# Kernel optimization log

Measured on AMD Instinct MI355X. Metric: run time of the kernel, lower is better.

Reference implementation:

```python
import jax, jax.numpy as jnp
import numpy as np

B, NPG, IN_DIM, H, E = 128, 500, 3, 128, 512000
N = B * NPG
NEG = -1e9  # stands in for -inf masked fill; exp underflows to exactly 0 in fp32
BN_EPS = 1e-5


def setup_inputs() -> dict:
    key = jax.random.key(0)
    ks = jax.random.split(key, 40)
    rn = lambda k, shape: (jax.random.normal(k, shape, jnp.float32) * 0.05)
    x = jax.random.normal(ks[0], (N, IN_DIM), jnp.float32)
    g = jax.random.randint(ks[1], (E,), 0, B)
    src = jax.random.randint(ks[2], (E,), 0, NPG) + g * NPG
    dst = jax.random.randint(ks[3], (E,), 0, NPG) + g * NPG
    edge_index = jnp.stack([src, dst]).astype(jnp.int32)
    batch = (jnp.arange(N) // NPG).astype(jnp.int32)
    feasible_mask = jax.random.uniform(ks[4], (B, NPG, NPG)) < 0.1
    feasible_mask = feasible_mask.at[:, 0, 0].set(True)  # >=1 feasible action/graph
    return dict(
        x=x, edge_index=edge_index, batch=batch, feasible_mask=feasible_mask,
        gin_W1_0=rn(ks[5], (IN_DIM, H)), gin_b1_0=jnp.zeros((H,), jnp.float32),
        gin_g_0=jnp.ones((H,), jnp.float32), gin_be_0=jnp.zeros((H,), jnp.float32),
        gin_W2_0=rn(ks[6], (H, H)), gin_b2_0=jnp.zeros((H,), jnp.float32),
        gin_W1=rn(ks[7], (3, H, H)), gin_b1=jnp.zeros((3, H), jnp.float32),
        gin_g=jnp.ones((3, H), jnp.float32), gin_be=jnp.zeros((3, H), jnp.float32),
        gin_W2=rn(ks[8], (3, H, H)), gin_b2=jnp.zeros((3, H), jnp.float32),
        pol_W1_0=rn(ks[9], (2 * H, H)), pol_b1_0=jnp.zeros((H,), jnp.float32),
        pol_W2_0=rn(ks[10], (H, H)), pol_b2_0=jnp.zeros((H,), jnp.float32),
        pol_W1=rn(ks[11], (2, H, H)), pol_b1=jnp.zeros((2, H), jnp.float32),
        pol_W2=rn(ks[12], (2, H, H)), pol_b2=jnp.zeros((2, H), jnp.float32),
    )


def _gin_conv(h, src, dst, deg, W1, b1, g, be, W2, b2):
    # mean-aggregate neighbors (self loops already in edge list), eps=0
    agg = jax.ops.segment_sum(h[src], dst, num_segments=N) / deg[:, None]
    z = (h + agg) @ W1 + b1
    mu = jnp.mean(z, axis=0)
    var = jnp.var(z, axis=0)  # biased var, as torch BN training mode
    z = (z - mu) * jax.lax.rsqrt(var + BN_EPS) * g + be
    return jax.nn.relu(z) @ W2 + b2


def reference(x, edge_index, batch, feasible_mask,
              gin_W1_0, gin_b1_0, gin_g_0, gin_be_0, gin_W2_0, gin_b2_0,
              gin_W1, gin_b1, gin_g, gin_be, gin_W2, gin_b2,
              pol_W1_0, pol_b1_0, pol_W2_0, pol_b2_0,
              pol_W1, pol_b1, pol_W2, pol_b2):
    # add self loops
    loop = jnp.arange(N, dtype=edge_index.dtype)
    src = jnp.concatenate([edge_index[0], loop])
    dst = jnp.concatenate([edge_index[1], loop])
    deg = jnp.maximum(jax.ops.segment_sum(jnp.ones_like(src, jnp.float32), dst, num_segments=N), 1.0)

    h = _gin_conv(x, src, dst, deg, gin_W1_0, gin_b1_0, gin_g_0, gin_be_0, gin_W2_0, gin_b2_0)
    node_pool = h
    graph_pool = jax.ops.segment_sum(h, batch, num_segments=B) / NPG
    for l in range(3):
        h = _gin_conv(h, src, dst, deg, gin_W1[l], gin_b1[l], gin_g[l], gin_be[l], gin_W2[l], gin_b2[l])
        node_pool = node_pool + h
        graph_pool = graph_pool + jax.ops.segment_sum(h, batch, num_segments=B) / NPG

    # augment node embeds with their graph embed (graphs contiguous, equal size)
    a = jnp.concatenate([node_pool, graph_pool[batch]], axis=-1).reshape(B, NPG, 2 * H)
    a = jnp.tanh(a @ pol_W1_0 + pol_b1_0) @ pol_W2_0 + pol_b2_0
    for l in range(2):
        a = jnp.tanh(a @ pol_W1[l] + pol_b1[l]) @ pol_W2[l] + pol_b2[l]

    scores = jnp.einsum('bnd,bmd->bnm', a, a)                 # [B, n, n]
    scores = jnp.where(feasible_mask, scores, NEG)
    flat = scores.reshape(B, NPG * NPG)
    logp_all = jax.nn.log_softmax(flat, axis=-1)
    actions_id = jax.random.categorical(jax.random.key(42), flat, axis=-1)  # [B]
    log_prob = jnp.take_along_axis(logp_all, actions_id[:, None], axis=1)[:, 0]
    return actions_id, log_prob
```

## Files before the change

### kernel.cpp

```cpp
#include <hip/hip_runtime.h>
#include <float.h>

#define NN 64000
#define BB 128
#define NPGc 500
#define EE 512000

#define SKW(c) ((c) + (((c)>>3)<<2))
#define LW 188

__device__ __forceinline__ unsigned rotl32(unsigned x, unsigned r){ return (x<<r)|(x>>(32u-r)); }

__device__ __forceinline__ unsigned threefry_bits(unsigned idx){
  unsigned x0 = 0u, x1 = idx;
  const unsigned ks0 = 0u, ks1 = 42u, ks2 = 0u ^ 42u ^ 0x1BD11BDAu;
  x0 += ks0; x1 += ks1;
#define RND(r) { x0 += x1; x1 = rotl32(x1, r); x1 ^= x0; }
  RND(13u) RND(15u) RND(26u) RND(6u)   x0 += ks1; x1 += ks2 + 1u;
  RND(17u) RND(29u) RND(16u) RND(24u)  x0 += ks2; x1 += ks0 + 2u;
  RND(13u) RND(15u) RND(26u) RND(6u)   x0 += ks0; x1 += ks1 + 3u;
  RND(17u) RND(29u) RND(16u) RND(24u)  x0 += ks1; x1 += ks2 + 4u;
  RND(13u) RND(15u) RND(26u) RND(6u)   x0 += ks2; x1 += ks0 + 5u;
#undef RND
  return x0 ^ x1;
}

__device__ __forceinline__ float gumbel_of(unsigned idx){
  unsigned bits = threefry_bits(idx);
  float f = __uint_as_float((bits >> 9) | 0x3f800000u) - 1.0f;
  const float TINY = 1.17549435e-38f;
  float u = fmaxf(TINY, f + TINY);
  return -logf(-logf(u));
}

__device__ __forceinline__ float fast_tanh(float x){
  return 1.0f - 2.0f/(__expf(2.0f*x) + 1.0f);
}

__global__ void maskdet_kernel(const unsigned* __restrict__ m, int* __restrict__ flag){
  if (threadIdx.x == 0){
    int isbool = 0;
    for (int i=0;i<256;i++){ if (m[i] > 1u){ isbool = 1; break; } }
    *flag = isbool;
  }
}

__global__ __launch_bounds__(256)
void maskprep_kernel(const unsigned char* __restrict__ mu8src, const int* __restrict__ mi32src,
                     const int* __restrict__ mflag, unsigned char* __restrict__ mn8,
                     unsigned char* __restrict__ mt8){
  __shared__ unsigned char tile[64][65];
  const int b = blockIdx.y;
  const int rt = blockIdx.x >> 3, ct = blockIdx.x & 7;
  const int t = threadIdx.x;
  const int lane = t & 63, rr = t >> 6;
  const int isbool = *mflag;
#pragma unroll
  for (int p=0;p<16;p++){
    int row = rt*64 + p*4 + rr;
    int col = ct*64 + lane;
    unsigned char v = 0;
    if (row < NPGc && col < NPGc){
      size_t off = (size_t)b*250000 + (size_t)row*500 + col;
      v = isbool ? mu8src[off] : (unsigned char)(mi32src[off] != 0);
      mn8[off] = v;
    }
    tile[p*4+rr][lane] = v;
  }
  __syncthreads();
#pragma unroll
  for (int p=0;p<16;p++){
    int orow = ct*64 + p*4 + rr;
    int ocol = rt*64 + lane;
    if (orow < NPGc && ocol < NPGc){
      size_t off = (size_t)b*250000 + (size_t)orow*500 + ocol;
      mt8[off] = tile[lane][p*4+rr];
    }
  }
}

__global__ void count_kernel(const int* __restrict__ dst, int* __restrict__ cnt){
  int e = blockIdx.x*256 + threadIdx.x;
  if (e < EE) atomicAdd(&cnt[dst[e]], 1);
}

__global__ void scanA_kernel(const int* __restrict__ cnt, int* __restrict__ bsum){
  __shared__ int red[256];
  int t = threadIdx.x;
  red[t] = cnt[blockIdx.x*256 + t];
  __syncthreads();
  for (int s=128;s>0;s>>=1){
    if (t < s) red[t] += red[t+s];
    __syncthreads();
  }
  if (t == 0) bsum[blockIdx.x] = red[0];
}

__global__ void scanB_kernel(const int* __restrict__ bsum, int* __restrict__ boff){
  if (threadIdx.x == 0){
    int run = 0;
    for (int i=0;i<250;i++){ boff[i] = run; run += bsum[i]; }
    boff[250] = run;
  }
}

__global__ void scanC_kernel(const int* __restrict__ cnt, const int* __restrict__ boff,
                             int* __restrict__ off, int* __restrict__ cur){
  __shared__ int red[256];
  int t = threadIdx.x;
  int n = blockIdx.x*256 + t;
  int v = cnt[n];
  red[t] = v;
  __syncthreads();
  for (int d=1; d<256; d<<=1){
    int x = (t >= d) ? red[t-d] : 0;
    __syncthreads();
    red[t] += x;
    __syncthreads();
  }
  int excl = red[t] - v + boff[blockIdx.x];
  off[n] = excl; cur[n] = excl;
  if (n == NN-1) off[NN] = excl + v;
}

__global__ void fill_kernel(const int* __restrict__ src, const int* __restrict__ dst,
                            int* __restrict__ cur, int* __restrict__ csr){
  int e = blockIdx.x*256 + threadIdx.x;
  if (e < EE){
    int d = dst[e];
    int p = atomicAdd(&cur[d], 1);
    csr[p] = src[e];
  }
}

__global__ __launch_bounds__(256)
void agg128_kernel(const float* __restrict__ h, const int* __restrict__ off,
                   const int* __restrict__ csr, const int* __restrict__ cnt,
                   float* __restrict__ xin){
  const int nb = gridDim.x;
  const int per = nb >> 3;
  int bid = (blockIdx.x % 8)*per + (blockIdx.x >> 3);
  int w = (bid*256 + (int)threadIdx.x) >> 6;
  int lane = threadIdx.x & 63;
  if (w >= NN) return;
  const float* hn = h + (size_t)w*128;
  float a0 = hn[lane], a1 = hn[lane+64];
  float s0 = a0, s1 = a1;
  int e0 = off[w], e1 = off[w+1];
  for (int e = e0; e < e1; ++e){
    int s = csr[e];
    const float* hs = h + (size_t)s*128;
    s0 += hs[lane]; s1 += hs[lane+64];
  }
  float di = 1.0f/(float)(cnt[w]+1);
  xin[(size_t)w*128 + lane]      = a0 + s0*di;
  xin[(size_t)w*128 + lane + 64] = a1 + s1*di;
}

__global__ __launch_bounds__(256)
void z0_kernel(const float* __restrict__ x, const int* __restrict__ off,
               const int* __restrict__ csr, const int* __restrict__ cnt,
               const float* __restrict__ W, const float* __restrict__ bias,
               float* __restrict__ z, float* __restrict__ stats){
  __shared__ float xr[192];
  __shared__ float ssum[128], ssq[128];
  int t = threadIdx.x;
  int row0 = blockIdx.x*64;
  if (t < 192){
    int nl = t/3, f = t - nl*3;
    int n = row0 + nl;
    float a = x[n*3+f];
    float s = a;
    int e1 = off[n+1];
    for (int e = off[n]; e < e1; ++e) s += x[csr[e]*3 + f];
    float di = 1.0f/(float)(cnt[n]+1);
    xr[t] = a + s*di;
  }
  if (t < 128){ ssum[t]=0.f; ssq[t]=0.f; }
  int f = t & 127, rg = t >> 7;
  float w0 = W[f], w1 = W[128+f], w2 = W[256+f], bb = bias[f];
  __syncthreads();
  float s = 0.f, q = 0.f;
  for (int i=0;i<32;i++){
    int r = rg*32 + i;
    float y = bb + xr[r*3]*w0 + xr[r*3+1]*w1 + xr[r*3+2]*w2;
    z[(size_t)(row0+r)*128 + f] = y;
    s += y; q += y*y;
  }
  atomicAdd(&ssum[f], s); atomicAdd(&ssq[f], q);
  __syncthreads();
  if (t < 128){ atomicAdd(&stats[t], ssum[t]); atomicAdd(&stats[128+t], ssq[t]); }
}

__global__ void bnfin_kernel(float* __restrict__ stats, const float* __restrict__ g,
                             const float* __restrict__ be, float* __restrict__ bnbuf){
  int f = threadIdx.x;
  float mu  = stats[f]     * (1.0f/NN);
  float var = stats[128+f] * (1.0f/NN) - mu*mu;
  float rsv = rsqrtf(var + 1e-5f);
  float sc  = g[f]*rsv;
  bnbuf[f]      = sc;
  bnbuf[128+f]  = be[f] - mu*sc;
  stats[f] = 0.f; stats[128+f] = 0.f;
}

template<int K, bool CATF, bool BNF, bool TANHF, bool STATSF, int POOLM>
__global__ __launch_bounds__(256, 2)
void linear_kernel(const float* X, const float* __restrict__ X2,
                   const float* __restrict__ W, const float* __restrict__ bias,
                   float* Y,
                   const float* __restrict__ bnsc, const float* __restrict__ bnsh,
                   float* __restrict__ stats, float* __restrict__ pool){
  __shared__ __align__(16) float xs[32][LW];
  __shared__ __align__(16) float ws[32][LW];
  __shared__ float ssum[128], ssq[128];
  const int t = threadIdx.x;
  const int row0 = blockIdx.x*128;
  const int cg = t & 15, rg = t >> 4;
  const int c0 = cg*8, r0 = rg*8;
  const int skr0 = SKW(r0), skc0 = SKW(c0);
  float acc[8][8];
#pragma unroll
  for (int r=0;r<8;r++)
#pragma unroll
    for (int c=0;c<8;c++) acc[r][c]=0.f;
  if (STATSF && t < 128){ ssum[t]=0.f; ssq[t]=0.f; }

  for (int kc=0; kc<K; kc+=32){
    __syncthreads();
#pragma unroll
    for (int i=0;i<4;i++){
      int task = t + 256*i;
      int n = task >> 3, k4 = task & 7;
      int gk = kc + k4*4;
      int row = row0 + n;
      float4 v;
      if (CATF){
        if (gk < 128) v = *(const float4*)(X  + (size_t)row*128 + gk);
        else          v = *(const float4*)(X2 + (size_t)(row/NPGc)*128 + (gk-128));
      } else {
        v = *(const float4*)(X + (size_t)row*K + gk);
      }
      if (BNF){
        float4 sc4 = *(const float4*)(bnsc + gk);
        float4 sh4 = *(const float4*)(bnsh + gk);
        v.x = fmaxf(0.f, v.x*sc4.x + sh4.x);
        v.y = fmaxf(0.f, v.y*sc4.y + sh4.y);
        v.z = fmaxf(0.f, v.z*sc4.z + sh4.z);
        v.w = fmaxf(0.f, v.w*sc4.w + sh4.w);
      }
      int ns = SKW(n);
      xs[k4*4+0][ns] = v.x; xs[k4*4+1][ns] = v.y;
      xs[k4*4+2][ns] = v.z; xs[k4*4+3][ns] = v.w;
    }
#pragma unroll
    for (int i=0;i<4;i++){
      int task = t + 256*i;
      int k = task >> 5, c4 = task & 31;
      float4 v = *(const float4*)(W + (size_t)(kc+k)*128 + c4*4);
      *(float4*)&ws[k][c4*4 + ((c4>>1)<<2)] = v;
    }
    __syncthreads();
#pragma unroll
    for (int k=0;k<32;k++){
      float4 xa = *(const float4*)&xs[k][skr0];
      float4 xb = *(const float4*)&xs[k][skr0+4];
      float4 wa = *(const float4*)&ws[k][skc0];
      float4 wb = *(const float4*)&ws[k][skc0+4];
      float xv[8] = {xa.x,xa.y,xa.z,xa.w,xb.x,xb.y,xb.z,xb.w};
      float wv[8] = {wa.x,wa.y,wa.z,wa.w,wb.x,wb.y,wb.z,wb.w};
#pragma unroll
      for (int r=0;r<8;r++)
#pragma unroll
        for (int c=0;c<8;c++)
          acc[r][c] += xv[r]*wv[c];
    }
  }
  float4 ba = *(const float4*)(bias + c0);
  float4 bb2 = *(const float4*)(bias + c0 + 4);
  float bv[8] = {ba.x,ba.y,ba.z,ba.w,bb2.x,bb2.y,bb2.z,bb2.w};
  float sc8[8], sq8[8];
#pragma unroll
  for (int c=0;c<8;c++){ sc8[c]=0.f; sq8[c]=0.f; }
#pragma unroll
  for (int r=0;r<8;r++){
    int n = row0 + r0 + r;
    float y[8];
#pragma unroll
    for (int c=0;c<8;c++){
      float v = acc[r][c] + bv[c];
      if (TANHF) v = fast_tanh(v);
      y[c] = v;
    }
    float4 y0; y0.x=y[0]; y0.y=y[1]; y0.z=y[2]; y0.w=y[3];
    float4 y1; y1.x=y[4]; y1.y=y[5]; y1.z=y[6]; y1.w=y[7];
    *(float4*)(Y + (size_t)n*128 + c0)     = y0;
    *(float4*)(Y + (size_t)n*128 + c0 + 4) = y1;
    if (POOLM == 1){
      *(float4*)(pool + (size_t)n*128 + c0)     = y0;
      *(float4*)(pool + (size_t)n*128 + c0 + 4) = y1;
    } else if (POOLM == 2){
      float4 p0 = *(const float4*)(pool + (size_t)n*128 + c0);
      float4 p1 = *(const float4*)(pool + (size_t)n*128 + c0 + 4);
      p0.x+=y[0]; p0.y+=y[1]; p0.z+=y[2]; p0.w+=y[3];
      p1.x+=y[4]; p1.y+=y[5]; p1.z+=y[6]; p1.w+=y[7];
      *(float4*)(pool + (size_t)n*128 + c0)     = p0;
      *(float4*)(pool + (size_t)n*128 + c0 + 4) = p1;
    }
    if (STATSF){
#pragma unroll
      for (int c=0;c<8;c++){ sc8[c]+=y[c]; sq8[c]+=y[c]*y[c]; }
    }
  }
  if (STATSF){
#pragma unroll
    for (int c=0;c<8;c++){
      atomicAdd(&ssum[c0+c], sc8[c]);
      atomicAdd(&ssq[c0+c],  sq8[c]);
    }
    __syncthreads();
    if (t < 128){
      atomicAdd(&stats[t],     ssum[t]);
      atomicAdd(&stats[128+t], ssq[t]);
    }
  }
}

__global__ __launch_bounds__(512)
void gpool_kernel(const float* __restrict__ pool, float* __restrict__ gpool){
  __shared__ float red[4][128];
  int b = blockIdx.x;
  int f = threadIdx.x & 127, part = threadIdx.x >> 7;
  const float* p = pool + (size_t)b*NPGc*128 + f;
  int rbeg = part*125, rend = rbeg + 125;
  float s = 0.f;
  for (int i=rbeg;i<rend;i++) s += p[(size_t)i*128];
  red[part][f] = s;
  __syncthreads();
  if (part == 0){
    float tot = ((red[0][f] + red[1][f]) + red[2][f]) + red[3][f];
    gpool[(size_t)b*128 + f] = tot * (1.0f/NPGc);
  }
}

#define QCAP 1024
#define NPAIR 36

__global__ __launch_bounds__(256)
void scores_tri_kernel(const float* __restrict__ A, const unsigned char* __restrict__ mn8,
                       const unsigned char* __restrict__ mt8, float* __restrict__ partials){
  __shared__ __align__(16) float as[128][68];
  __shared__ __align__(16) float bs[32][68];
  __shared__ float qs[QCAP];
  __shared__ int   qi[QCAP];
  __shared__ int   qcnt;
  float* rm  = qs;
  float* rs_ = qs + 256;
  float* rv  = qs + 512;
  float* rsc = qs + 768;
  int*   ri  = qi;
  const int t = threadIdx.x;
  const int lane = t & 63;
  const int xcd = blockIdx.x & 7;
  const int within = blockIdx.x >> 3;
  const int b = xcd*16 + within/NPAIR;
  int pidx = within % NPAIR, tn = 0;
  while (pidx >= 8 - tn){ pidx -= 8 - tn; tn++; }
  const int tm = tn + pidx;
  const int pair = within % NPAIR;
  const bool diag = (tn == tm);
  const int n0 = tn*64, m0 = tm*64;
  const int cgc = t & 15, rgc = t >> 4;
  const int r0_ = rgc*4, c0 = cgc*4;
  const float* Ab = A + (size_t)b*NPGc*128;
  const unsigned gbase = (unsigned)b*250000u;
  if (t == 0) qcnt = 0;

#pragma unroll
  for (int i=0;i<32;i++){
    int idx = t + 256*i;
    int k = idx & 127, r = idx >> 7;
    int n = n0 + r;
    as[k][r] = (n < NPGc) ? Ab[(size_t)n*128 + k] : 0.f;
  }

  float acc[4][4];
#pragma unroll
  for (int i2=0;i2<4;i2++)
#pragma unroll
    for (int j=0;j<4;j++) acc[i2][j]=0.f;

  for (int kc=0;kc<4;kc++){
    __syncthreads();
#pragma unroll
    for (int i=0;i<8;i++){
      int idx = t + 256*i;
      int kk = idx & 31, c = idx >> 5;
      int m = m0 + c;
      bs[kk][c] = (m < NPGc) ? Ab[(size_t)m*128 + kc*32 + kk] : 0.f;
    }
    __syncthreads();
#pragma unroll
    for (int kk=0;kk<32;kk++){
      float4 av = *(const float4*)&as[kc*32+kk][r0_];
      float4 bv4 = *(const float4*)&bs[kk][c0];
      float a_[4] = {av.x,av.y,av.z,av.w};
      float b_[4] = {bv4.x,bv4.y,bv4.z,bv4.w};
#pragma unroll
      for (int i2=0;i2<4;i2++)
#pragma unroll
        for (int j=0;j<4;j++)
          acc[i2][j] += a_[i2]*b_[j];
    }
  }

  float mrun = -1e30f, srun = 0.f, bval = -FLT_MAX, bsc = 0.f;
  int bidx = 0x7FFFFFFF;
  const int mbase = m0 + c0;
  const bool colok = (mbase < NPGc);
#pragma unroll
  for (int i2=0;i2<4;i2++){
    int n = n0 + r0_ + i2;
    bool rowok = colok && (n < NPGc);
    bool fn[4] = {false,false,false,false};
    bool fm[4] = {false,false,false,false};
    if (rowok){
      size_t moff = (size_t)b*250000 + (size_t)n*500 + (size_t)mbase;
      uchar4 mk = *(const uchar4*)(mn8 + moff);
      fn[0]=mk.x!=0; fn[1]=mk.y!=0; fn[2]=mk.z!=0; fn[3]=mk.w!=0;
      uchar4 tk = *(const uchar4*)(mt8 + moff);
      fm[0]=tk.x!=0; fm[1]=tk.y!=0; fm[2]=tk.z!=0; fm[3]=tk.w!=0;
    }
    float cntj[4], sj[4];
    bool pn[4], pm[4];
#pragma unroll
    for (int j=0;j<4;j++){
      int m = mbase + j;
      bool mok = rowok && (m < NPGc);
      bool keep = mok && (!diag || m >= n);
      bool isde = (n == m);
      float cnt = 0.f; bool a1=false, a2=false;
      if (keep){
        if (isde){ cnt = fn[j] ? 1.f : 0.f; a1 = fn[j]; }
        else { cnt = (fn[j]?1.f:0.f) + (fm[j]?1.f:0.f); a1 = fn[j]; a2 = fm[j]; }
      }
      cntj[j]=cnt; pn[j]=a1; pm[j]=a2;
      sj[j] = (cnt > 0.f) ? acc[i2][j] : -1e30f;
    }
    float tmx = fmaxf(fmaxf(sj[0],sj[1]), fmaxf(sj[2],sj[3]));
    float nm = fmaxf(mrun, tmx);
    float add = 0.f;
#pragma unroll
    for (int j=0;j<4;j++) add += cntj[j]*__expf(sj[j] - nm);
    srun = srun*__expf(mrun - nm) + add;
    mrun = nm;
#pragma unroll
    for (int j=0;j<4;j++){
      int m = mbase + j;
      float s = acc[i2][j];
#pragma unroll
      for (int d=0;d<2;d++){
        bool want = d ? pm[j] : pn[j];
        unsigned long long mb = __ballot(want);
        if (mb){
          int cntw = __popcll(mb);
          int pos  = __popcll(mb & ((1ull<<lane)-1ull));
          int basew = 0;
          if (lane == 0) basew = atomicAdd(&qcnt, cntw);
          basew = __shfl(basew, 0);
          if (want){
            int lidx = d ? (m*500 + n) : (n*500 + m);
            int slot = basew + pos;
            if (slot < QCAP){ qs[slot] = s; qi[slot] = lidx; }
            else {
              float g = gumbel_of(gbase + (unsigned)lidx);
              float val = s + g;
              if (val > bval || (val == bval && lidx < bidx)){ bval = val; bidx = lidx; bsc = s; }
            }
          }
        }
      }
    }
  }
  __syncthreads();
  int qn = qcnt; if (qn > QCAP) qn = QCAP;
  for (int i = t; i < qn; i += 256){
    float s = qs[i]; int idx = qi[i];
    float g = gumbel_of(gbase + (unsigned)idx);
    float val = s + g;
    if (val > bval || (val == bval && idx < bidx)){ bval = val; bidx = idx; bsc = s; }
  }
  __syncthreads();
  rm[t]=mrun; rs_[t]=srun; rv[t]=bval; ri[t]=bidx; rsc[t]=bsc;
  __syncthreads();
  for (int offr=128; offr>0; offr>>=1){
    if (t < offr){
      float m1 = rm[t], s1 = rs_[t];
      float m2 = rm[t+offr], s2 = rs_[t+offr];
      float M = fmaxf(m1, m2);
      float S = s1*expf(m1-M) + s2*expf(m2-M);
      rm[t] = M; rs_[t] = S;
      float v2 = rv[t+offr]; int i2_ = ri[t+offr];
      if (v2 > rv[t] || (v2 == rv[t] && i2_ < ri[t])){ rv[t]=v2; ri[t]=i2_; rsc[t]=rsc[t+offr]; }
    }
    __syncthreads();
  }
  if (t == 0){
    float* p = partials + ((size_t)b*NPAIR + pair)*8;
    p[0]=rm[0]; p[1]=rs_[0]; p[2]=rv[0]; p[3]=(float)ri[0]; p[4]=rsc[0];
  }
}

__global__ void finalize_kernel(const float* __restrict__ partials, float* __restrict__ out){
  int b = threadIdx.x;
  float M = -1e30f, S = 0.f, BV = -FLT_MAX, BS = 0.f;
  int BI = 0x7FFFFFFF;
  for (int tp=0; tp<NPAIR; tp++){
    const float* p = partials + ((size_t)b*NPAIR + tp)*8;
    float m = p[0], s = p[1], v = p[2]; int i = (int)p[3]; float sc2 = p[4];
    float nM = fmaxf(M, m);
    S = S*expf(M-nM) + s*expf(m-nM);
    M = nM;
    if (v > BV || (v == BV && i < BI)){ BV = v; BI = i; BS = sc2; }
  }
  out[b]      = (float)BI;
  out[BB + b] = BS - (M + logf(S));
}

extern "C" void kernel_launch(void* const* d_in, const int* in_sizes, int n_in,
                              void* d_out, int out_size, void* d_ws, size_t ws_size,
                              hipStream_t stream){
  const float* x        = (const float*)d_in[0];
  const int*   eidx     = (const int*)d_in[1];
  const void*  maskp    = d_in[3];
  const float* gin_W1_0 = (const float*)d_in[4];
  const float* gin_b1_0 = (const float*)d_in[5];
  const float* gin_g_0  = (const float*)d_in[6];
  const float* gin_be_0 = (const float*)d_in[7];
  const float* gin_W2_0 = (const float*)d_in[8];
  const float* gin_b2_0 = (const float*)d_in[9];
  const float* gin_W1   = (const float*)d_in[10];
  const float* gin_b1   = (const float*)d_in[11];
  const float* gin_g    = (const float*)d_in[12];
  const float* gin_be   = (const float*)d_in[13];
  const float* gin_W2   = (const float*)d_in[14];
  const float* gin_b2   = (const float*)d_in[15];
  const float* pol_W1_0 = (const float*)d_in[16];
  const float* pol_b1_0 = (const float*)d_in[17];
  const float* pol_W2_0 = (const float*)d_in[18];
  const float* pol_b2_0 = (const float*)d_in[19];
  const float* pol_W1   = (const float*)d_in[20];
  const float* pol_b1   = (const float*)d_in[21];
  const float* pol_W2   = (const float*)d_in[22];
  const float* pol_b2   = (const float*)d_in[23];
  float* out = (float*)d_out;

  char* p = (char*)d_ws;
  auto carve = [&](size_t bytes) -> void* {
    void* r = (void*)p; p += (bytes + 255) & ~(size_t)255; return r;
  };
  float* hbuf  = (float*)carve((size_t)NN*128*4);
  float* xin   = (float*)carve((size_t)NN*128*4);
  float* pool  = (float*)carve((size_t)NN*128*4);
  float* gpool = (float*)carve((size_t)BB*128*4);
  float* stats = (float*)carve(256*4);
  float* bnbuf = (float*)carve(256*4);
  float* partials = (float*)carve((size_t)BB*NPAIR*8*4);
  int* cnt  = (int*)carve((size_t)NN*4);
  int* off  = (int*)carve((size_t)(NN+1)*4);
  int* cur  = (int*)carve((size_t)NN*4);
  int* csr  = (int*)carve((size_t)EE*4);
  int* bsum = (int*)carve(256*4);
  int* boff = (int*)carve(256*4);
  int* mflag = (int*)carve(256);
  unsigned char* mn8 = (unsigned char*)carve((size_t)BB*250000);
  unsigned char* mt8 = (unsigned char*)carve((size_t)BB*250000);

  const int* srcp = eidx;
  const int* dstp = eidx + EE;

  maskdet_kernel<<<1, 64, 0, stream>>>((const unsigned*)maskp, mflag);
  {
    dim3 mg(64, BB);
    maskprep_kernel<<<mg, 256, 0, stream>>>((const unsigned char*)maskp, (const int*)maskp,
                                            mflag, mn8, mt8);
  }

  hipMemsetAsync(cnt, 0, (size_t)NN*4, stream);
  count_kernel<<<(EE+255)/256, 256, 0, stream>>>(dstp, cnt);
  scanA_kernel<<<NN/256, 256, 0, stream>>>(cnt, bsum);
  scanB_kernel<<<1, 64, 0, stream>>>(bsum, boff);
  scanC_kernel<<<NN/256, 256, 0, stream>>>(cnt, boff, off, cur);
  fill_kernel<<<(EE+255)/256, 256, 0, stream>>>(srcp, dstp, cur, csr);

  hipMemsetAsync(stats, 0, 256*4, stream);
  z0_kernel<<<NN/64, 256, 0, stream>>>(x, off, csr, cnt, gin_W1_0, gin_b1_0, xin, stats);
  bnfin_kernel<<<1, 128, 0, stream>>>(stats, gin_g_0, gin_be_0, bnbuf);
  linear_kernel<128,false,true,false,false,1><<<NN/128, 256, 0, stream>>>(
      xin, nullptr, gin_W2_0, gin_b2_0, hbuf, bnbuf, bnbuf+128, nullptr, pool);

  for (int l=0; l<3; l++){
    agg128_kernel<<<NN/4, 256, 0, stream>>>(hbuf, off, csr, cnt, xin);
    linear_kernel<128,false,false,false,true,0><<<NN/128, 256, 0, stream>>>(
        xin, nullptr, gin_W1 + (size_t)l*16384, gin_b1 + l*128, xin,
        nullptr, nullptr, stats, nullptr);
    bnfin_kernel<<<1, 128, 0, stream>>>(stats, gin_g + l*128, gin_be + l*128, bnbuf);
    linear_kernel<128,false,true,false,false,2><<<NN/128, 256, 0, stream>>>(
        xin, nullptr, gin_W2 + (size_t)l*16384, gin_b2 + l*128, hbuf,
        bnbuf, bnbuf+128, nullptr, pool);
  }

  gpool_kernel<<<BB, 512, 0, stream>>>(pool, gpool);
  linear_kernel<256,true,false,true,false,0><<<NN/128, 256, 0, stream>>>(
      pool, gpool, pol_W1_0, pol_b1_0, hbuf, nullptr, nullptr, nullptr, nullptr);
  linear_kernel<128,false,false,false,false,0><<<NN/128, 256, 0, stream>>>(
      hbuf, nullptr, pol_W2_0, pol_b2_0, xin, nullptr, nullptr, nullptr, nullptr);
  linear_kernel<128,false,false,true,false,0><<<NN/128, 256, 0, stream>>>(
      xin, nullptr, pol_W1, pol_b1, hbuf, nullptr, nullptr, nullptr, nullptr);
  linear_kernel<128,false,false,false,false,0><<<NN/128, 256, 0, stream>>>(
      hbuf, nullptr, pol_W2, pol_b2, xin, nullptr, nullptr, nullptr, nullptr);
  linear_kernel<128,false,false,true,false,0><<<NN/128, 256, 0, stream>>>(
      xin, nullptr, pol_W1 + 16384, pol_b1 + 128, hbuf, nullptr, nullptr, nullptr, nullptr);
  linear_kernel<128,false,false,false,false,0><<<NN/128, 256, 0, stream>>>(
      hbuf, nullptr, pol_W2 + 16384, pol_b2 + 128, xin, nullptr, nullptr, nullptr, nullptr);

  scores_tri_kernel<<<8*16*NPAIR, 256, 0, stream>>>(xin, mn8, mt8, partials);
  finalize_kernel<<<1, BB, 0, stream>>>(partials, out);
}
```

Measured before the change: 1.325 ms.

## Fold BN finalize and mask detection into consumers, parallelize scan, unroll gather

Removes the separate mask-detect and BN-finalize launches. Mask type detection now happens inside each maskprep block with a block-wide OR, and BN scale and shift are computed per block into shared memory from per-layer stats buffers. The single-thread block-offset scan becomes a parallel shared-memory scan. The neighbor gather loop is unrolled by four for more loads in flight, and the scores queue push switches from a wave-aggregated ballot to per-lane atomics on the shared counter. The last change may add atomic contention, and every block now redoes the BN finalize math.

```diff
diff --git a/kernel.cpp b/kernel.cpp
--- a/kernel.cpp
+++ b/kernel.cpp
@@ -37,24 +37,16 @@
   return 1.0f - 2.0f/(__expf(2.0f*x) + 1.0f);
 }
 
-__global__ void maskdet_kernel(const unsigned* __restrict__ m, int* __restrict__ flag){
-  if (threadIdx.x == 0){
-    int isbool = 0;
-    for (int i=0;i<256;i++){ if (m[i] > 1u){ isbool = 1; break; } }
-    *flag = isbool;
-  }
-}
-
 __global__ __launch_bounds__(256)
 void maskprep_kernel(const unsigned char* __restrict__ mu8src, const int* __restrict__ mi32src,
-                     const int* __restrict__ mflag, unsigned char* __restrict__ mn8,
-                     unsigned char* __restrict__ mt8){
+                     unsigned char* __restrict__ mn8, unsigned char* __restrict__ mt8){
   __shared__ unsigned char tile[64][65];
   const int b = blockIdx.y;
   const int rt = blockIdx.x >> 3, ct = blockIdx.x & 7;
   const int t = threadIdx.x;
   const int lane = t & 63, rr = t >> 6;
-  const int isbool = *mflag;
+  int mybad = (((const unsigned*)mi32src)[t] > 1u) ? 1 : 0;
+  int isbool = __syncthreads_or(mybad);
 #pragma unroll
   for (int p=0;p<16;p++){
     int row = rt*64 + p*4 + rr;
@@ -97,11 +89,19 @@
 }
 
 __global__ void scanB_kernel(const int* __restrict__ bsum, int* __restrict__ boff){
-  if (threadIdx.x == 0){
-    int run = 0;
-    for (int i=0;i<250;i++){ boff[i] = run; run += bsum[i]; }
-    boff[250] = run;
-  }
+  __shared__ int red[256];
+  int t = threadIdx.x;
+  int v = (t < 250) ? bsum[t] : 0;
+  red[t] = v;
+  __syncthreads();
+  for (int d=1; d<256; d<<=1){
+    int x = (t >= d) ? red[t-d] : 0;
+    __syncthreads();
+    red[t] += x;
+    __syncthreads();
+  }
+  if (t < 250) boff[t] = red[t] - v;
+  if (t == 249) boff[250] = red[t];
 }
 
 __global__ void scanC_kernel(const int* __restrict__ cnt, const int* __restrict__ boff,
@@ -147,7 +147,23 @@
   float a0 = hn[lane], a1 = hn[lane+64];
   float s0 = a0, s1 = a1;
   int e0 = off[w], e1 = off[w+1];
-  for (int e = e0; e < e1; ++e){
+  int e = e0;
+  for (; e + 4 <= e1; e += 4){
+    int sA = csr[e], sB = csr[e+1], sC = csr[e+2], sD = csr[e+3];
+    const float* pA = h + (size_t)sA*128;
+    const float* pB = h + (size_t)sB*128;
+    const float* pC = h + (size_t)sC*128;
+    const float* pD = h + (size_t)sD*128;
+    float a0A = pA[lane], a1A = pA[lane+64];
+    float a0B = pB[lane], a1B = pB[lane+64];
+    float a0C = pC[lane], a1C = pC[lane+64];
+    float a0D = pD[lane], a1D = pD[lane+64];
+    s0 += a0A; s1 += a1A;
+    s0 += a0B; s1 += a1B;
+    s0 += a0C; s1 += a1C;
+    s0 += a0D; s1 += a1D;
+  }
+  for (; e < e1; ++e){
     int s = csr[e];
     const float* hs = h + (size_t)s*128;
     s0 += hs[lane]; s1 += hs[lane+64];
@@ -192,28 +208,18 @@
   if (t < 128){ atomicAdd(&stats[t], ssum[t]); atomicAdd(&stats[128+t], ssq[t]); }
 }
 
-__global__ void bnfin_kernel(float* __restrict__ stats, const float* __restrict__ g,
-                             const float* __restrict__ be, float* __restrict__ bnbuf){
-  int f = threadIdx.x;
-  float mu  = stats[f]     * (1.0f/NN);
-  float var = stats[128+f] * (1.0f/NN) - mu*mu;
-  float rsv = rsqrtf(var + 1e-5f);
-  float sc  = g[f]*rsv;
-  bnbuf[f]      = sc;
-  bnbuf[128+f]  = be[f] - mu*sc;
-  stats[f] = 0.f; stats[128+f] = 0.f;
-}
-
 template<int K, bool CATF, bool BNF, bool TANHF, bool STATSF, int POOLM>
 __global__ __launch_bounds__(256, 2)
 void linear_kernel(const float* X, const float* __restrict__ X2,
                    const float* __restrict__ W, const float* __restrict__ bias,
                    float* Y,
-                   const float* __restrict__ bnsc, const float* __restrict__ bnsh,
-                   float* __restrict__ stats, float* __restrict__ pool){
+                   const float* __restrict__ statsIn, const float* __restrict__ gam,
+                   const float* __restrict__ bet,
+                   float* __restrict__ statsOut, float* __restrict__ pool){
   __shared__ __align__(16) float xs[32][LW];
   __shared__ __align__(16) float ws[32][LW];
   __shared__ float ssum[128], ssq[128];
+  __shared__ __align__(16) float bnsc_s[128], bnsh_s[128];
   const int t = threadIdx.x;
   const int row0 = blockIdx.x*128;
   const int cg = t & 15, rg = t >> 4;
@@ -225,6 +231,14 @@
 #pragma unroll
     for (int c=0;c<8;c++) acc[r][c]=0.f;
   if (STATSF && t < 128){ ssum[t]=0.f; ssq[t]=0.f; }
+  if (BNF && t < 128){
+    float mu  = statsIn[t]     * (1.0f/NN);
+    float var = statsIn[128+t] * (1.0f/NN) - mu*mu;
+    float rsv = rsqrtf(var + 1e-5f);
+    float sc  = gam[t]*rsv;
+    bnsc_s[t] = sc;
+    bnsh_s[t] = bet[t] - mu*sc;
+  }
 
   for (int kc=0; kc<K; kc+=32){
     __syncthreads();
@@ -242,8 +256,8 @@
         v = *(const float4*)(X + (size_t)row*K + gk);
       }
       if (BNF){
-        float4 sc4 = *(const float4*)(bnsc + gk);
-        float4 sh4 = *(const float4*)(bnsh + gk);
+        float4 sc4 = *(const float4*)(bnsc_s + gk);
+        float4 sh4 = *(const float4*)(bnsh_s + gk);
         v.x = fmaxf(0.f, v.x*sc4.x + sh4.x);
         v.y = fmaxf(0.f, v.y*sc4.y + sh4.y);
         v.z = fmaxf(0.f, v.z*sc4.z + sh4.z);
@@ -320,8 +334,8 @@
     }
     __syncthreads();
     if (t < 128){
-      atomicAdd(&stats[t],     ssum[t]);
-      atomicAdd(&stats[128+t], ssq[t]);
+      atomicAdd(&statsOut[t],     ssum[t]);
+      atomicAdd(&statsOut[128+t], ssq[t]);
     }
   }
 }
@@ -360,7 +374,6 @@
   float* rsc = qs + 768;
   int*   ri  = qi;
   const int t = threadIdx.x;
-  const int lane = t & 63;
   const int xcd = blockIdx.x & 7;
   const int within = blockIdx.x >> 3;
   const int b = xcd*16 + within/NPAIR;
@@ -457,20 +470,14 @@
 #pragma unroll
     for (int j=0;j<4;j++){
       int m = mbase + j;
-      float s = acc[i2][j];
-#pragma unroll
-      for (int d=0;d<2;d++){
-        bool want = d ? pm[j] : pn[j];
-        unsigned long long mb = __ballot(want);
-        if (mb){
-          int cntw = __popcll(mb);
-          int pos  = __popcll(mb & ((1ull<<lane)-1ull));
-          int basew = 0;
-          if (lane == 0) basew = atomicAdd(&qcnt, cntw);
-          basew = __shfl(basew, 0);
-          if (want){
+      if (pn[j] || pm[j]){
+        float s = acc[i2][j];
+#pragma unroll
+        for (int d=0;d<2;d++){
+          bool doit = d ? pm[j] : pn[j];
+          if (doit){
             int lidx = d ? (m*500 + n) : (n*500 + m);
-            int slot = basew + pos;
+            int slot = atomicAdd(&qcnt, 1);
             if (slot < QCAP){ qs[slot] = s; qi[slot] = lidx; }
             else {
               float g = gumbel_of(gbase + (unsigned)lidx);
@@ -563,8 +570,7 @@
   float* xin   = (float*)carve((size_t)NN*128*4);
   float* pool  = (float*)carve((size_t)NN*128*4);
   float* gpool = (float*)carve((size_t)BB*128*4);
-  float* stats = (float*)carve(256*4);
-  float* bnbuf = (float*)carve(256*4);
+  float* stats = (float*)carve(4*256*4);
   float* partials = (float*)carve((size_t)BB*NPAIR*8*4);
   int* cnt  = (int*)carve((size_t)NN*4);
   int* off  = (int*)carve((size_t)(NN+1)*4);
@@ -572,57 +578,54 @@
   int* csr  = (int*)carve((size_t)EE*4);
   int* bsum = (int*)carve(256*4);
   int* boff = (int*)carve(256*4);
-  int* mflag = (int*)carve(256);
   unsigned char* mn8 = (unsigned char*)carve((size_t)BB*250000);
   unsigned char* mt8 = (unsigned char*)carve((size_t)BB*250000);
 
   const int* srcp = eidx;
   const int* dstp = eidx + EE;
 
-  maskdet_kernel<<<1, 64, 0, stream>>>((const unsigned*)maskp, mflag);
   {
     dim3 mg(64, BB);
     maskprep_kernel<<<mg, 256, 0, stream>>>((const unsigned char*)maskp, (const int*)maskp,
-                                            mflag, mn8, mt8);
+                                            mn8, mt8);
   }
 
   hipMemsetAsync(cnt, 0, (size_t)NN*4, stream);
+  hipMemsetAsync(stats, 0, 4*256*4, stream);
   count_kernel<<<(EE+255)/256, 256, 0, stream>>>(dstp, cnt);
   scanA_kernel<<<NN/256, 256, 0, stream>>>(cnt, bsum);
-  scanB_kernel<<<1, 64, 0, stream>>>(bsum, boff);
+  scanB_kernel<<<1, 256, 0, stream>>>(bsum, boff);
   scanC_kernel<<<NN/256, 256, 0, stream>>>(cnt, boff, off, cur);
   fill_kernel<<<(EE+255)/256, 256, 0, stream>>>(srcp, dstp, cur, csr);
 
-  hipMemsetAsync(stats, 0, 256*4, stream);
   z0_kernel<<<NN/64, 256, 0, stream>>>(x, off, csr, cnt, gin_W1_0, gin_b1_0, xin, stats);
-  bnfin_kernel<<<1, 128, 0, stream>>>(stats, gin_g_0, gin_be_0, bnbuf);
   linear_kernel<128,false,true,false,false,1><<<NN/128, 256, 0, stream>>>(
-      xin, nullptr, gin_W2_0, gin_b2_0, hbuf, bnbuf, bnbuf+128, nullptr, pool);
+      xin, nullptr, gin_W2_0, gin_b2_0, hbuf, stats, gin_g_0, gin_be_0, nullptr, pool);
 
   for (int l=0; l<3; l++){
+    float* st = stats + (l+1)*256;
     agg128_kernel<<<NN/4, 256, 0, stream>>>(hbuf, off, csr, cnt, xin);
     linear_kernel<128,false,false,false,true,0><<<NN/128, 256, 0, stream>>>(
         xin, nullptr, gin_W1 + (size_t)l*16384, gin_b1 + l*128, xin,
-        nullptr, nullptr, stats, nullptr);
-    bnfin_kernel<<<1, 128, 0, stream>>>(stats, gin_g + l*128, gin_be + l*128, bnbuf);
+        nullptr, nullptr, nullptr, st, nullptr);
     linear_kernel<128,false,true,false,false,2><<<NN/128, 256, 0, stream>>>(
         xin, nullptr, gin_W2 + (size_t)l*16384, gin_b2 + l*128, hbuf,
-        bnbuf, bnbuf+128, nullptr, pool);
+        st, gin_g + l*128, gin_be + l*128, nullptr, pool);
   }
 
   gpool_kernel<<<BB, 512, 0, stream>>>(pool, gpool);
   linear_kernel<256,true,false,true,false,0><<<NN/128, 256, 0, stream>>>(
-      pool, gpool, pol_W1_0, pol_b1_0, hbuf, nullptr, nullptr, nullptr, nullptr);
+      pool, gpool, pol_W1_0, pol_b1_0, hbuf, nullptr, nullptr, nullptr, nullptr, nullptr);
   linear_kernel<128,false,false,false,false,0><<<NN/128, 256, 0, stream>>>(
-      hbuf, nullptr, pol_W2_0, pol_b2_0, xin, nullptr, nullptr, nullptr, nullptr);
+      hbuf, nullptr, pol_W2_0, pol_b2_0, xin, nullptr, nullptr, nullptr, nullptr, nullptr);
   linear_kernel<128,false,false,true,false,0><<<NN/128, 256, 0, stream>>>(
-      xin, nullptr, pol_W1, pol_b1, hbuf, nullptr, nullptr, nullptr, nullptr);
+      xin, nullptr, pol_W1, pol_b1, hbuf, nullptr, nullptr, nullptr, nullptr, nullptr);
   linear_kernel<128,false,false,false,false,0><<<NN/128, 256, 0, stream>>>(
-      hbuf, nullptr, pol_W2, pol_b2, xin, nullptr, nullptr, nullptr, nullptr);
+      hbuf, nullptr, pol_W2, pol_b2, xin, nullptr, nullptr, nullptr, nullptr, nullptr);
   linear_kernel<128,false,false,true,false,0><<<NN/128, 256, 0, stream>>>(
-      xin, nullptr, pol_W1 + 16384, pol_b1 + 128, hbuf, nullptr, nullptr, nullptr, nullptr);
+      xin, nullptr, pol_W1 + 16384, pol_b1 + 128, hbuf, nullptr, nullptr, nullptr, nullptr, nullptr);
   linear_kernel<128,false,false,false,false,0><<<NN/128, 256, 0, stream>>>(
-      hbuf, nullptr, pol_W2 + 16384, pol_b2 + 128, xin, nullptr, nullptr, nullptr, nullptr);
+      hbuf, nullptr, pol_W2 + 16384, pol_b2 + 128, xin, nullptr, nullptr, nullptr, nullptr, nullptr);
 
   scores_tri_kernel<<<8*16*NPAIR, 256, 0, stream>>>(xin, mn8, mt8, partials);
   finalize_kernel<<<1, BB, 0, stream>>>(partials, out);
```

Result: faster. 1.206 ms (-9.0%).
